# Optimization experiments

Measured on AMD Instinct MI355X. Metric: run time of the kernel, lower is better.

Reference implementation:

```python
import jax, jax.numpy as jnp
import numpy as np

N = 50000      # nodes
E = 400000     # edges
HID = 128      # hidden_size
L = 3          # num_att_layer
K = 9          # rbf_size
H = 4          # heads
C = HID // H   # out_channels per head (32)
G = 512        # graphs in batch
CUTOFF = 10.0


def _rbf(D):
    # ExponentialRBF: softplus(softplus_inverse(x)) == x, so centers/widths are the raw values
    centers = jnp.linspace(1.0, float(np.exp(-CUTOFF)), K)          # (K,)
    width = (0.5 / ((1.0 - np.exp(-CUTOFF)) / K)) ** 2              # scalar
    x = D / CUTOFF
    x3 = x ** 3
    x4 = x3 * x
    x5 = x4 * x
    cut = jnp.where(x < 1.0, 1.0 - 6.0 * x5 + 15.0 * x4 - 10.0 * x3, 0.0)
    return cut[:, None] * jnp.exp(-width * (jnp.exp(-D)[:, None] - centers) ** 2)  # (E,K)


def _ln(x, g, b):
    mu = jnp.mean(x, axis=-1, keepdims=True)
    var = jnp.var(x, axis=-1, keepdims=True)
    return (x - mu) / jnp.sqrt(var + 1e-5) * g + b


def _seg_softmax(logits, seg, n):
    # numerically stable softmax over edges grouped by target node
    m = jax.ops.segment_max(logits, seg, num_segments=n)
    e = jnp.exp(logits - m[seg])
    s = jax.ops.segment_sum(e, seg, num_segments=n)
    return e / s[seg]


def setup_inputs() -> dict:
    key = jax.random.key(0)
    ks = jax.random.split(key, 32)
    s = 1.0 / np.sqrt(HID)
    se = 1.0 / np.sqrt(K + 1)
    sb = 1.0 / np.sqrt(3 * HID)
    nrm = jax.random.normal
    inp = {
        "h": nrm(ks[0], (N, HID), jnp.float32),
        "pos": nrm(ks[1], (N, 3), jnp.float32) * 3.0,
        "edge_weight": jax.random.uniform(ks[2], (E,), jnp.float32),
        "Wq": nrm(ks[3], (L, HID, HID)) * s,   "bq": nrm(ks[4], (L, HID)) * 0.01,
        "Wk": nrm(ks[5], (L, HID, HID)) * s,   "bk": nrm(ks[6], (L, HID)) * 0.01,
        "Wv": nrm(ks[7], (L, HID, HID)) * s,   "bv": nrm(ks[8], (L, HID)) * 0.01,
        "We": nrm(ks[9], (L, K + 1, HID)) * se,
        "Wskip": nrm(ks[10], (L, HID, HID)) * s, "bskip": nrm(ks[11], (L, HID)) * 0.01,
        "Wbeta": nrm(ks[12], (L, 3 * HID, 1)) * sb,
        "Wffn1": nrm(ks[13], (L, HID, HID)) * s, "bffn1": nrm(ks[14], (L, HID)) * 0.01,
        "Wffn2": nrm(ks[15], (L, HID, HID)) * s, "bffn2": nrm(ks[16], (L, HID)) * 0.01,
        "Wffn3": nrm(ks[17], (L, HID, HID)) * s, "bffn3": nrm(ks[18], (L, HID)) * 0.01,
        "ln_g": jnp.ones((HID,), jnp.float32),
        "ln_b": jnp.zeros((HID,), jnp.float32),
        "Wo1": nrm(ks[19], (HID, HID)) * s, "bo1": nrm(ks[20], (HID,)) * 0.01,
        "Wo2": nrm(ks[21], (HID, 1)) * s,   "bo2": nrm(ks[22], (1,)) * 0.01,
        "edge_index": jax.random.randint(ks[23], (2, E), 0, N),
        "batch": jnp.sort(jax.random.randint(ks[24], (N,), 0, G)),
    }
    return inp


def reference(h, pos, edge_weight, Wq, bq, Wk, bk, Wv, bv, We, Wskip, bskip, Wbeta,
              Wffn1, bffn1, Wffn2, bffn2, Wffn3, bffn3, ln_g, ln_b, Wo1, bo1, Wo2, bo2,
              edge_index, batch):
    sp = jax.nn.softplus
    n = h.shape[0]
    src, dst = edge_index[0], edge_index[1]  # source j -> target i
    D = jnp.linalg.norm(pos[dst] - pos[src], axis=-1)              # (E,)
    efeat = jnp.concatenate([_rbf(D), edge_weight[:, None]], -1)   # (E, K+1)
    inv_sqrt_c = 1.0 / np.sqrt(C)

    for i in range(L):
        hn = _ln(h, ln_g, ln_b)
        q = (hn @ Wq[i] + bq[i]).reshape(n, H, C)
        k = (hn @ Wk[i] + bk[i]).reshape(n, H, C)
        v = (hn @ Wv[i] + bv[i]).reshape(n, H, C)
        ea = (efeat @ We[i]).reshape(-1, H, C)                     # (E,H,C)
        kj = k[src] + ea
        alpha = jnp.einsum('ehc,ehc->eh', q[dst], kj) * inv_sqrt_c  # (E,H)
        alpha = _seg_softmax(alpha, dst, n)
        # dropout p=0.5 is a no-op in eval mode
        msg = (v[src] + ea) * alpha[:, :, None]
        out = jax.ops.segment_sum(msg, dst, num_segments=n).reshape(n, H * C)
        x_r = hn @ Wskip[i] + bskip[i]
        beta = jax.nn.sigmoid(jnp.concatenate([out, x_r, out - x_r], -1) @ Wbeta[i])
        out = beta * x_r + (1.0 - beta) * out
        h = hn + sp(out)
        hn2 = _ln(h, ln_g, ln_b)
        f = sp(hn2 @ Wffn1[i] + bffn1[i])
        f = sp(f @ Wffn2[i] + bffn2[i])
        f = sp(f @ Wffn3[i] + bffn3[i])
        h = hn2 + f

    pooled = jax.ops.segment_sum(h, batch, num_segments=G)          # (G, HID)
    return sp(pooled @ Wo1 + bo1) @ Wo2 + bo2                       # (G, 1)
```

## Files before the change

kernel.cpp:

```cpp
#include <hip/hip_runtime.h>
#include <hip/hip_bf16.h>
#include <math.h>

#define HID 128
#define KRBF 9
#define NLAYER 3
#define IPAD 136

typedef __attribute__((ext_vector_type(8))) short bf16x8;
typedef __attribute__((ext_vector_type(4))) float f32x4;

__device__ __forceinline__ float sp_(float x){ return fmaxf(x,0.f) + log1pf(expf(-fabsf(x))); }
__device__ __forceinline__ float sigm_(float x){ return 1.f/(1.f+expf(-x)); }
__device__ __forceinline__ float b2f(short s){
  union{unsigned u; float f;} x; x.u = ((unsigned)(unsigned short)s)<<16; return x.f;
}
__device__ __forceinline__ short f2bs(float x){
  __hip_bfloat16 b = __float2bfloat16(x);
  return *reinterpret_cast<short*>(&b);
}
__device__ __forceinline__ float wsum64(float v){
  #pragma unroll
  for(int m=1;m<64;m<<=1) v += __shfl_xor(v,m,64);
  return v;
}
__device__ __forceinline__ float wsum16(float v){
  #pragma unroll
  for(int m=1;m<16;m<<=1) v += __shfl_xor(v,m,64);
  return v;
}
__device__ __forceinline__ int lb_(const int* __restrict__ a, int n, int key){
  int lo=0, hi=n;
  while(lo<hi){ int mid=(lo+hi)>>1; if(a[mid]<key) lo=mid+1; else hi=mid; }
  return lo;
}

__global__ void count_dst(const int* __restrict__ ei, int* __restrict__ counts, int E){
  int e = blockIdx.x*256+threadIdx.x;
  if(e<E) atomicAdd(&counts[ei[E+e]],1);
}
__global__ void scan1(const int* __restrict__ counts, int* __restrict__ tmp,
                      int* __restrict__ bsums, int N){
  __shared__ int lds[256];
  int t = threadIdx.x; int idx = blockIdx.x*256+t;
  int v = (idx<N)? counts[idx]:0;
  lds[t]=v; __syncthreads();
  for(int off=1;off<256;off<<=1){
    int x = (t>=off)? lds[t-off]:0;
    __syncthreads();
    lds[t]+=x; __syncthreads();
  }
  if(idx<N) tmp[idx]=lds[t];
  if(t==255) bsums[blockIdx.x]=lds[255];
}
__global__ void scan2(const int* __restrict__ bsums, int* __restrict__ boffs, int nb){
  __shared__ int lds[256];
  int t=threadIdx.x;
  int v = (t<nb)? bsums[t]:0;
  lds[t]=v; __syncthreads();
  for(int off=1;off<256;off<<=1){
    int x=(t>=off)?lds[t-off]:0;
    __syncthreads();
    lds[t]+=x; __syncthreads();
  }
  if(t<nb) boffs[t] = lds[t]-v;
}
__global__ void finalize_rs(const int* __restrict__ tmp, const int* __restrict__ boffs,
                            int* __restrict__ row_start, int N){
  int idx = blockIdx.x*256+threadIdx.x;
  if(idx<N) row_start[idx+1] = tmp[idx] + boffs[idx>>8];
  if(idx==0) row_start[0]=0;
}
__global__ void csr_scatter(const int* __restrict__ ei, const int* __restrict__ rowst,
                            int* __restrict__ counts2, int* __restrict__ csr, int E){
  int e = blockIdx.x*256+threadIdx.x;
  if(e>=E) return;
  int d = ei[E+e];
  int p = rowst[d] + atomicAdd(&counts2[d],1);
  csr[p] = e;
}
__global__ void sort_seg(const int* __restrict__ rowst, int* __restrict__ csr, int N){
  int n = blockIdx.x*256+threadIdx.x;
  if(n>=N) return;
  int lo=rowst[n], hi=rowst[n+1];
  for(int i=lo+1;i<hi;i++){
    int v=csr[i]; int j=i-1;
    while(j>=lo && csr[j]>v){ csr[j+1]=csr[j]; j--; }
    csr[j+1]=v;
  }
}
__global__ void edge_feat(const float* __restrict__ pos, const float* __restrict__ ew,
                          const int* __restrict__ ei, const int* __restrict__ csr,
                          float* __restrict__ efs, int* __restrict__ esrc, int E){
  int p = blockIdx.x*256 + threadIdx.x;
  if(p>=E) return;
  int e = csr[p];
  int s = ei[e], d = ei[E+e];
  float dx = pos[d*3+0]-pos[s*3+0];
  float dy = pos[d*3+1]-pos[s*3+1];
  float dz = pos[d*3+2]-pos[s*3+2];
  float D = sqrtf(dx*dx+dy*dy+dz*dz);
  float x = D*0.1f;
  float cut = 0.f;
  if(x < 1.f){ float x3=x*x*x, x4=x3*x, x5=x4*x; cut = 1.f - 6.f*x5 + 15.f*x4 - 10.f*x3; }
  float ed = expf(-D);
  const double e10 = 4.5399929762484854e-05;
  const float step  = (float)((e10 - 1.0)/8.0);
  const float width = (float)((4.5/(1.0-e10))*(4.5/(1.0-e10)));
  float r12[12];
  #pragma unroll
  for(int k=0;k<KRBF;k++){
    float c = 1.0f + k*step;
    float dd = ed - c;
    r12[k] = cut*expf(-width*dd*dd);
  }
  r12[9] = ew[e]; r12[10]=0.f; r12[11]=0.f;
  float* o = efs + (size_t)p*12;
  *(float4*)&o[0] = *(float4*)&r12[0];
  *(float4*)&o[4] = *(float4*)&r12[4];
  *(float4*)&o[8] = *(float4*)&r12[8];
  esrc[p] = s;
}

__global__ void pack_w(const float* __restrict__ Wq, const float* __restrict__ Wk,
                       const float* __restrict__ Wv, const float* __restrict__ Wsk,
                       const float* __restrict__ bq, const float* __restrict__ bk,
                       const float* __restrict__ bv, const float* __restrict__ bsk,
                       const float* __restrict__ We,
                       const float* __restrict__ W1, const float* __restrict__ W2,
                       const float* __restrict__ W3,
                       __hip_bfloat16* __restrict__ Wqkvs, float* __restrict__ bqkvs,
                       __hip_bfloat16* __restrict__ Wffn){
  int idx = blockIdx.x*256 + threadIdx.x;
  const int QT = NLAYER*5*16384;
  const int FT = NLAYER*3*16384;
  const int BT = NLAYER*640;
  if(idx < QT){
    int l = idx / (5*16384);
    int rem = idx - l*(5*16384);
    int cb = rem >> 14;
    int t = rem & 16383;
    int j = t&7; int lane = (t>>3)&63; int blk = t>>9;
    int kc = blk>>3, nj = blk&7, ql = lane>>4, il = lane&15;
    int k = kc*32 + ql*8 + j;
    int gcol = cb*128 + il*8 + nj;
    float v = 0.f;
    if(gcol < 512){
      const float* src = (gcol<128)?Wq:((gcol<256)?Wk:((gcol<384)?Wv:Wsk));
      v = src[(size_t)l*16384 + k*128 + (gcol&127)];
    } else if(gcol < 552){
      int jj = gcol-512; int h=jj/10; int r=jj-10*h;
      const float* wq = Wq + (size_t)l*16384 + k*128;
      const float* we = We + (size_t)l*1280 + r*128;
      float acc=0.f;
      #pragma unroll 8
      for(int c=32*h;c<32*h+32;c++) acc = fmaf(wq[c], we[c], acc);
      v = acc;
    }
    Wqkvs[idx] = __float2bfloat16(v);
  } else if(idx < QT+FT){
    int r0 = idx - QT;
    int l = r0 / (3*16384);
    int rem = r0 - l*(3*16384);
    int f = rem >> 14;
    int t = rem & 16383;
    int j = t&7; int lane = (t>>3)&63; int blk = t>>9;
    int kc = blk>>3, nj = blk&7, ql = lane>>4, il = lane&15;
    int k = kc*32 + ql*8 + j;
    int gcol = il*8 + nj;
    const float* src = (f==0)?W1:((f==1)?W2:W3);
    Wffn[r0] = __float2bfloat16(src[(size_t)l*16384 + k*128 + gcol]);
  } else if(idx < QT+FT+BT){
    int j = idx - QT - FT;
    int l = j/640; int col = j - l*640;
    float v = 0.f;
    if(col<512){
      const float* src = (col<128)?bq:((col<256)?bk:((col<384)?bv:bsk));
      v = src[l*128 + (col&127)];
    } else if(col<552){
      int jj=col-512; int h=jj/10; int r=jj-10*h;
      const float* bqp = bq + l*128;
      const float* we = We + (size_t)l*1280 + r*128;
      float acc=0.f;
      for(int c=32*h;c<32*h+32;c++) acc = fmaf(bqp[c], we[c], acc);
      v = acc;
    }
    bqkvs[j] = v;
  }
}

__global__ void ln_node(const float* __restrict__ h, const float* __restrict__ g,
                        const float* __restrict__ b, __hip_bfloat16* __restrict__ hn, int N){
  int n = blockIdx.x*4 + (threadIdx.x>>6);
  if(n>=N) return;
  int lane = threadIdx.x & 63;
  int c = 2*lane;
  float2 v = *(const float2*)&h[(size_t)n*HID + c];
  float s1 = wsum64(v.x+v.y);
  float s2 = wsum64(v.x*v.x+v.y*v.y);
  float mu = s1*(1.f/HID);
  float var = s2*(1.f/HID) - mu*mu;
  float rs = rsqrtf(var + 1e-5f);
  __hip_bfloat162 o;
  o.x = __float2bfloat16((v.x-mu)*rs*g[c]   + b[c]);
  o.y = __float2bfloat16((v.y-mu)*rs*g[c+1] + b[c+1]);
  *(__hip_bfloat162*)&hn[(size_t)n*HID + c] = o;
}

__global__ __launch_bounds__(256) void gemm_qkvs(
    const __hip_bfloat16* __restrict__ A, const __hip_bfloat16* __restrict__ Wt,
    const float* __restrict__ bias,
    __hip_bfloat16* __restrict__ qsO, __hip_bfloat16* __restrict__ kvO,
    float* __restrict__ qwO, int N){
  __shared__ __hip_bfloat16 WsF[16384];
  int row0 = blockIdx.y*128;
  int cb = blockIdx.x;
  int tid = threadIdx.x;
  {
    const __hip_bfloat16* Wp = Wt + (size_t)cb*16384;
    #pragma unroll
    for(int i=0;i<8;i++){
      int o = (tid + 256*i)*8;
      *(float4*)&WsF[o] = *(const float4*)&Wp[o];
    }
  }
  int lane = tid&63;
  int m0 = (tid>>6)*32;
  int ql = lane>>4, il = lane&15;
  bf16x8 af[2][4];
  #pragma unroll
  for(int mi=0;mi<2;mi++){
    int r = row0 + m0 + mi*16 + il;
    r = (r < N) ? r : (N-1);
    const __hip_bfloat16* ap = A + (size_t)r*128 + ql*8;
    #pragma unroll
    for(int kc=0;kc<4;kc++) af[mi][kc] = *(const bf16x8*)(ap + kc*32);
  }
  __syncthreads();
  f32x4 acc[2][8];
  #pragma unroll
  for(int mi=0;mi<2;mi++)
    #pragma unroll
    for(int nj=0;nj<8;nj++) acc[mi][nj] = (f32x4){0.f,0.f,0.f,0.f};
  #pragma unroll
  for(int kc=0;kc<4;kc++){
    #pragma unroll
    for(int nj=0;nj<8;nj++){
      bf16x8 bb = *(bf16x8*)&WsF[((kc*8+nj)*64 + lane)*8];
      #pragma unroll
      for(int mi=0;mi<2;mi++)
        acc[mi][nj] = __builtin_amdgcn_mfma_f32_16x16x32_bf16(af[mi][kc], bb, acc[mi][nj], 0,0,0);
    }
  }
  float bl8[8];
  {
    float4 b0 = *(const float4*)&bias[cb*128 + il*8];
    float4 b1 = *(const float4*)&bias[cb*128 + il*8 + 4];
    bl8[0]=b0.x; bl8[1]=b0.y; bl8[2]=b0.z; bl8[3]=b0.w;
    bl8[4]=b1.x; bl8[5]=b1.y; bl8[6]=b1.z; bl8[7]=b1.w;
  }
  #pragma unroll
  for(int mi=0;mi<2;mi++){
    #pragma unroll
    for(int r=0;r<4;r++){
      int rr = row0 + m0 + mi*16 + ql*4 + r;
      if(rr >= N) continue;
      if(cb < 4){
        bf16x8 o;
        #pragma unroll
        for(int nj=0;nj<8;nj++) o[nj] = f2bs(acc[mi][nj][r] + bl8[nj]);
        __hip_bfloat16* dst;
        if(cb==0)      dst = qsO + (size_t)rr*256 + il*8;
        else if(cb==1) dst = kvO + (size_t)rr*256 + il*8;
        else if(cb==2) dst = kvO + (size_t)rr*256 + 128 + il*8;
        else           dst = qsO + (size_t)rr*256 + 128 + il*8;
        *(bf16x8*)dst = o;
      } else if(il < 5){
        #pragma unroll
        for(int nj=0;nj<8;nj++){
          int g = il*8 + nj;
          int h = g/10, rb = g - 10*h;
          qwO[(size_t)rr*48 + h*12 + rb] = acc[mi][nj][r] + bl8[nj];
        }
      }
    }
  }
}

__global__ __launch_bounds__(256) void attn_fused4(
    const __hip_bfloat16* __restrict__ qs, const __hip_bfloat16* __restrict__ kvb,
    const float* __restrict__ qwb, const float* __restrict__ efs,
    const int* __restrict__ esrc, const float* __restrict__ WeL,
    const int* __restrict__ rowst, const __hip_bfloat16* __restrict__ hn,
    const float* __restrict__ Wb, const float* __restrict__ lng,
    const float* __restrict__ lnb, __hip_bfloat16* __restrict__ hn2, int N){
  int n = blockIdx.x*4 + (threadIdx.x>>6);
  if(n>=N) return;
  int lane = threadIdx.x & 63;
  int eg = lane>>4, sl = lane&15;
  int c8 = sl*8, hd = sl>>2;
  const __hip_bfloat16* rowq = qs + (size_t)n*256;
  float q8[8];
  {
    bf16x8 qv = *(const bf16x8*)&rowq[c8];
    #pragma unroll
    for(int j=0;j<8;j++) q8[j] = b2f(qv[j]);
  }
  const float* qwp = qwb + (size_t)n*48 + hd*12;
  float4 qa = *(const float4*)qwp;
  float4 qb = *(const float4*)(qwp+4);
  float2 qc = *(const float2*)(qwp+8);
  float QW[10] = {qa.x,qa.y,qa.z,qa.w,qb.x,qb.y,qb.z,qb.w,qc.x,qc.y};
  int lo = rowst[n], hi = rowst[n+1];
  float ssum = 0.f, a8[8], S[10];
  #pragma unroll
  for(int j=0;j<8;j++) a8[j]=0.f;
  #pragma unroll
  for(int r=0;r<10;r++) S[r]=0.f;
  int i = lo + eg;
  if(i < hi){
    int s = esrc[i];
    const __hip_bfloat16* kr = kvb + (size_t)s*256;
    bf16x8 kc = *(const bf16x8*)&kr[c8];
    bf16x8 vc = *(const bf16x8*)&kr[128 + c8];
    const float* ef = efs + (size_t)i*12;
    float4 e0 = *(const float4*)&ef[0];
    float4 e1 = *(const float4*)&ef[4];
    float2 e2 = *(const float2*)&ef[8];
    while(true){
      int inext = i + 4;
      bool more = inext < hi;
      bf16x8 kn = kc, vn = vc;
      float4 f0 = e0, f1 = e1; float2 f2 = e2;
      if(more){
        int s2 = esrc[inext];
        const __hip_bfloat16* kr2 = kvb + (size_t)s2*256;
        kn = *(const bf16x8*)&kr2[c8];
        vn = *(const bf16x8*)&kr2[128 + c8];
        const float* ef2 = efs + (size_t)inext*12;
        f0 = *(const float4*)&ef2[0];
        f1 = *(const float4*)&ef2[4];
        f2 = *(const float2*)&ef2[8];
      }
      float d = 0.f;
      #pragma unroll
      for(int j=0;j<8;j++) d = fmaf(q8[j], b2f(kc[j]), d);
      d += __shfl_xor(d,1,64); d += __shfl_xor(d,2,64);
      float lg = d;
      lg = fmaf(e0.x,QW[0],lg); lg = fmaf(e0.y,QW[1],lg);
      lg = fmaf(e0.z,QW[2],lg); lg = fmaf(e0.w,QW[3],lg);
      lg = fmaf(e1.x,QW[4],lg); lg = fmaf(e1.y,QW[5],lg);
      lg = fmaf(e1.z,QW[6],lg); lg = fmaf(e1.w,QW[7],lg);
      lg = fmaf(e2.x,QW[8],lg); lg = fmaf(e2.y,QW[9],lg);
      lg *= 0.17677669529663687f;
      lg = fminf(lg, 80.f);
      float w = __expf(lg);
      ssum += w;
      #pragma unroll
      for(int j=0;j<8;j++) a8[j] = fmaf(w, b2f(vc[j]), a8[j]);
      S[0]=fmaf(w,e0.x,S[0]); S[1]=fmaf(w,e0.y,S[1]); S[2]=fmaf(w,e0.z,S[2]);
      S[3]=fmaf(w,e0.w,S[3]); S[4]=fmaf(w,e1.x,S[4]); S[5]=fmaf(w,e1.y,S[5]);
      S[6]=fmaf(w,e1.z,S[6]); S[7]=fmaf(w,e1.w,S[7]); S[8]=fmaf(w,e2.x,S[8]);
      S[9]=fmaf(w,e2.y,S[9]);
      if(!more) break;
      kc = kn; vc = vn; e0 = f0; e1 = f1; e2 = f2;
      i = inext;
    }
  }
  float o8[8];
  #pragma unroll
  for(int j=0;j<8;j++) o8[j]=a8[j];
  #pragma unroll
  for(int r=0;r<10;r++){
    float s=S[r];
    float4 wa = *(const float4*)&WeL[r*128+c8];
    float4 wb = *(const float4*)&WeL[r*128+c8+4];
    o8[0]=fmaf(s,wa.x,o8[0]); o8[1]=fmaf(s,wa.y,o8[1]);
    o8[2]=fmaf(s,wa.z,o8[2]); o8[3]=fmaf(s,wa.w,o8[3]);
    o8[4]=fmaf(s,wb.x,o8[4]); o8[5]=fmaf(s,wb.y,o8[5]);
    o8[6]=fmaf(s,wb.z,o8[6]); o8[7]=fmaf(s,wb.w,o8[7]);
  }
  #pragma unroll
  for(int m=16;m<64;m<<=1){
    ssum += __shfl_xor(ssum,m,64);
    #pragma unroll
    for(int j=0;j<8;j++) o8[j] += __shfl_xor(o8[j],m,64);
  }
  float inv = (hi>lo)? 1.f/ssum : 0.f;
  #pragma unroll
  for(int j=0;j<8;j++) o8[j] *= inv;
  float xr8[8];
  {
    bf16x8 xv = *(const bf16x8*)&rowq[128 + c8];
    #pragma unroll
    for(int j=0;j<8;j++) xr8[j] = b2f(xv[j]);
  }
  float pb = 0.f;
  {
    float4 a0=*(const float4*)&Wb[c8],     a1=*(const float4*)&Wb[c8+4];
    float4 b0=*(const float4*)&Wb[128+c8], b1=*(const float4*)&Wb[128+c8+4];
    float4 c0=*(const float4*)&Wb[256+c8], c1=*(const float4*)&Wb[256+c8+4];
    float wb0[8]={a0.x,a0.y,a0.z,a0.w,a1.x,a1.y,a1.z,a1.w};
    float wb1[8]={b0.x,b0.y,b0.z,b0.w,b1.x,b1.y,b1.z,b1.w};
    float wb2[8]={c0.x,c0.y,c0.z,c0.w,c1.x,c1.y,c1.z,c1.w};
    #pragma unroll
    for(int j=0;j<8;j++)
      pb += o8[j]*wb0[j] + xr8[j]*wb1[j] + (o8[j]-xr8[j])*wb2[j];
  }
  pb = wsum16(pb);
  float beta = sigm_(pb);
  float h8[8], s1=0.f, s2=0.f;
  {
    bf16x8 hv = *(const bf16x8*)&hn[(size_t)n*128 + c8];
    #pragma unroll
    for(int j=0;j<8;j++){
      float u = beta*xr8[j] + (1.f-beta)*o8[j];
      float x = b2f(hv[j]) + sp_(u);
      h8[j]=x; s1+=x; s2+=x*x;
    }
  }
  s1 = wsum16(s1); s2 = wsum16(s2);
  float mu = s1*(1.f/128.f);
  float var = s2*(1.f/128.f) - mu*mu;
  float rsg = rsqrtf(var + 1e-5f);
  if(eg==0){
    float4 g0=*(const float4*)&lng[c8], g1=*(const float4*)&lng[c8+4];
    float4 bb0=*(const float4*)&lnb[c8], bb1=*(const float4*)&lnb[c8+4];
    float g8[8]={g0.x,g0.y,g0.z,g0.w,g1.x,g1.y,g1.z,g1.w};
    float lb8[8]={bb0.x,bb0.y,bb0.z,bb0.w,bb1.x,bb1.y,bb1.z,bb1.w};
    bf16x8 o;
    #pragma unroll
    for(int j=0;j<8;j++) o[j] = f2bs((h8[j]-mu)*rsg*g8[j] + lb8[j]);
    *(bf16x8*)&hn2[(size_t)n*128 + c8] = o;
  }
}

__global__ __launch_bounds__(256) void ffn_fused(
    const __hip_bfloat16* __restrict__ hn2, const __hip_bfloat16* __restrict__ Wf,
    const float* __restrict__ b1, const float* __restrict__ b2,
    const float* __restrict__ b3, const float* __restrict__ lng,
    const float* __restrict__ lnb, float* __restrict__ hout,
    __hip_bfloat16* __restrict__ hnout, int N){
  __shared__ __hip_bfloat16 WsF[16384];
  __shared__ __hip_bfloat16 inter[2][64][IPAD];
  int row0 = blockIdx.x*64;
  int tid = threadIdx.x, lane = tid&63, wv = tid>>6;
  int ql = lane>>4, il = lane&15;

  auto stage = [&](const __hip_bfloat16* Wp){
    #pragma unroll
    for(int i=0;i<8;i++){
      int o = (tid + 256*i)*8;
      *(float4*)&WsF[o] = *(const float4*)&Wp[o];
    }
  };
  auto loadbias = [&](const float* bp, float* bl8){
    float4 x0 = *(const float4*)&bp[il*8];
    float4 x1 = *(const float4*)&bp[il*8+4];
    bl8[0]=x0.x; bl8[1]=x0.y; bl8[2]=x0.z; bl8[3]=x0.w;
    bl8[4]=x1.x; bl8[5]=x1.y; bl8[6]=x1.z; bl8[7]=x1.w;
  };

  f32x4 acc[8];
  bf16x8 af[4];
  stage(Wf);
  {
    int r = row0 + wv*16 + il;
    r = (r<N)? r : (N-1);
    const __hip_bfloat16* ap = hn2 + (size_t)r*128 + ql*8;
    #pragma unroll
    for(int kc=0;kc<4;kc++) af[kc] = *(const bf16x8*)(ap + kc*32);
  }
  __syncthreads();
  #pragma unroll
  for(int nj=0;nj<8;nj++) acc[nj] = (f32x4){0.f,0.f,0.f,0.f};
  #pragma unroll
  for(int kc=0;kc<4;kc++)
    #pragma unroll
    for(int nj=0;nj<8;nj++){
      bf16x8 bb = *(bf16x8*)&WsF[((kc*8+nj)*64 + lane)*8];
      acc[nj] = __builtin_amdgcn_mfma_f32_16x16x32_bf16(af[kc], bb, acc[nj], 0,0,0);
    }
  {
    float bl8[8]; loadbias(b1, bl8);
    #pragma unroll
    for(int r=0;r<4;r++){
      int lr = wv*16 + ql*4 + r;
      bf16x8 o;
      #pragma unroll
      for(int nj=0;nj<8;nj++) o[nj] = f2bs(sp_(acc[nj][r] + bl8[nj]));
      *(bf16x8*)&inter[0][lr][il*8] = o;
    }
  }
  __syncthreads();
  stage(Wf + 16384);
  #pragma unroll
  for(int kc=0;kc<4;kc++) af[kc] = *(bf16x8*)&inter[0][wv*16+il][ql*8 + kc*32];
  __syncthreads();
  #pragma unroll
  for(int nj=0;nj<8;nj++) acc[nj] = (f32x4){0.f,0.f,0.f,0.f};
  #pragma unroll
  for(int kc=0;kc<4;kc++)
    #pragma unroll
    for(int nj=0;nj<8;nj++){
      bf16x8 bb = *(bf16x8*)&WsF[((kc*8+nj)*64 + lane)*8];
      acc[nj] = __builtin_amdgcn_mfma_f32_16x16x32_bf16(af[kc], bb, acc[nj], 0,0,0);
    }
  {
    float bl8[8]; loadbias(b2, bl8);
    #pragma unroll
    for(int r=0;r<4;r++){
      int lr = wv*16 + ql*4 + r;
      bf16x8 o;
      #pragma unroll
      for(int nj=0;nj<8;nj++) o[nj] = f2bs(sp_(acc[nj][r] + bl8[nj]));
      *(bf16x8*)&inter[1][lr][il*8] = o;
    }
  }
  __syncthreads();
  stage(Wf + 2*16384);
  #pragma unroll
  for(int kc=0;kc<4;kc++) af[kc] = *(bf16x8*)&inter[1][wv*16+il][ql*8 + kc*32];
  __syncthreads();
  #pragma unroll
  for(int nj=0;nj<8;nj++) acc[nj] = (f32x4){0.f,0.f,0.f,0.f};
  #pragma unroll
  for(int kc=0;kc<4;kc++)
    #pragma unroll
    for(int nj=0;nj<8;nj++){
      bf16x8 bb = *(bf16x8*)&WsF[((kc*8+nj)*64 + lane)*8];
      acc[nj] = __builtin_amdgcn_mfma_f32_16x16x32_bf16(af[kc], bb, acc[nj], 0,0,0);
    }
  {
    float bl8[8]; loadbias(b3, bl8);
    float lg8[8], lb8[8];
    loadbias(lng, lg8); loadbias(lnb, lb8);
    #pragma unroll
    for(int r=0;r<4;r++){
      int rr = row0 + wv*16 + ql*4 + r;
      if(rr >= N) continue;
      bf16x8 rv = *(const bf16x8*)&hn2[(size_t)rr*128 + il*8];
      float t8[8], s1=0.f, s2=0.f;
      #pragma unroll
      for(int nj=0;nj<8;nj++){
        float x = sp_(acc[nj][r] + bl8[nj]) + b2f(rv[nj]);
        t8[nj]=x; s1+=x; s2+=x*x;
      }
      s1 = wsum16(s1); s2 = wsum16(s2);
      float mu = s1*(1.f/128.f);
      float var = s2*(1.f/128.f) - mu*mu;
      float rsg = rsqrtf(var + 1e-5f);
      *(float4*)&hout[(size_t)rr*128 + il*8]     = make_float4(t8[0],t8[1],t8[2],t8[3]);
      *(float4*)&hout[(size_t)rr*128 + il*8 + 4] = make_float4(t8[4],t8[5],t8[6],t8[7]);
      bf16x8 o;
      #pragma unroll
      for(int nj=0;nj<8;nj++) o[nj] = f2bs((t8[nj]-mu)*rsg*lg8[nj] + lb8[nj]);
      *(bf16x8*)&hnout[(size_t)rr*128 + il*8] = o;
    }
  }
}

__global__ void pool_head(const float* __restrict__ h, const int* __restrict__ batch,
                          const float* __restrict__ Wo1, const float* __restrict__ bo1,
                          const float* __restrict__ Wo2, const float* __restrict__ bo2,
                          float* __restrict__ out, int N){
  int gid = blockIdx.x;
  int t = threadIdx.x;
  int lo = lb_(batch, N, gid), hi = lb_(batch, N, gid+1);
  __shared__ float pl[128];
  __shared__ float red[128];
  float s = 0.f;
  for(int i=lo;i<hi;i++) s += h[(size_t)i*HID + t];
  pl[t] = s;
  __syncthreads();
  float acc = bo1[t];
  for(int c=0;c<128;c++) acc = fmaf(pl[c], Wo1[c*HID+t], acc);
  red[t] = sp_(acc)*Wo2[t];
  __syncthreads();
  for(int off=64;off>0;off>>=1){
    if(t<off) red[t]+=red[t+off];
    __syncthreads();
  }
  if(t==0) out[gid] = red[0] + bo2[0];
}

extern "C" void kernel_launch(void* const* d_in, const int* in_sizes, int n_in,
                              void* d_out, int out_size, void* d_ws, size_t ws_size,
                              hipStream_t stream){
  const float* h_in = (const float*)d_in[0];
  const float* pos  = (const float*)d_in[1];
  const float* ew   = (const float*)d_in[2];
  const float* Wq = (const float*)d_in[3];  const float* bq = (const float*)d_in[4];
  const float* Wk = (const float*)d_in[5];  const float* bk = (const float*)d_in[6];
  const float* Wv = (const float*)d_in[7];  const float* bv = (const float*)d_in[8];
  const float* We = (const float*)d_in[9];
  const float* Wsk= (const float*)d_in[10]; const float* bsk=(const float*)d_in[11];
  const float* Wbeta=(const float*)d_in[12];
  const float* W1=(const float*)d_in[13]; const float* b1=(const float*)d_in[14];
  const float* W2=(const float*)d_in[15]; const float* b2=(const float*)d_in[16];
  const float* W3=(const float*)d_in[17]; const float* b3=(const float*)d_in[18];
  const float* lng=(const float*)d_in[19]; const float* lnb=(const float*)d_in[20];
  const float* Wo1=(const float*)d_in[21]; const float* bo1=(const float*)d_in[22];
  const float* Wo2=(const float*)d_in[23]; const float* bo2=(const float*)d_in[24];
  const int* ei    = (const int*)d_in[25];
  const int* batch = (const int*)d_in[26];
  int N = in_sizes[0]/HID;
  int E = in_sizes[2];
  int G = out_size;
  float* out = (float*)d_out;

  char* ws = (char*)d_ws;
  size_t off=0;
  auto alloc=[&](size_t bytes)->char*{
    char* p = ws + off;
    off = (off + bytes + 255) & ~(size_t)255;
    return p;
  };
  float* efs   =(float*)alloc((size_t)E*12*4);
  int* esrc    =(int*)  alloc((size_t)E*4);
  int* csr     =(int*)  alloc((size_t)E*4);
  int* counts  =(int*)  alloc((size_t)N*4);
  int* counts2 =(int*)  alloc((size_t)N*4);
  int* rowst   =(int*)  alloc((size_t)(N+1)*4);
  int* tmp     =(int*)  alloc((size_t)N*4);
  int* bsums   =(int*)  alloc(256*4);
  int* boffs   =(int*)  alloc(256*4);
  __hip_bfloat16* hn   =(__hip_bfloat16*)alloc((size_t)N*HID*2);
  __hip_bfloat16* hn2  =(__hip_bfloat16*)alloc((size_t)N*HID*2);
  __hip_bfloat16* qsb  =(__hip_bfloat16*)alloc((size_t)N*256*2);
  __hip_bfloat16* kvb  =(__hip_bfloat16*)alloc((size_t)N*256*2);
  float* qwb   =(float*)alloc((size_t)N*48*4);
  float* hcur  =(float*)alloc((size_t)N*HID*4);
  __hip_bfloat16* Wqkvs_t =(__hip_bfloat16*)alloc((size_t)NLAYER*5*16384*2);
  __hip_bfloat16* Wffn_t  =(__hip_bfloat16*)alloc((size_t)NLAYER*3*16384*2);
  float* bqkvs =(float*)alloc((size_t)NLAYER*640*4);

  int ebl = (E+255)/256;
  int nb  = (N+255)/256;
  int nwb = (N+3)/4;
  int nrb128 = (N+127)/128;
  int nrb64  = (N+63)/64;
  dim3 gqkvs(5, nrb128);

  hipMemsetAsync(counts, 0, (size_t)N*4, stream);
  hipMemsetAsync(counts2,0, (size_t)N*4, stream);
  count_dst<<<ebl,256,0,stream>>>(ei,counts,E);
  scan1<<<nb,256,0,stream>>>(counts,tmp,bsums,N);
  scan2<<<1,256,0,stream>>>(bsums,boffs,nb);
  finalize_rs<<<nb,256,0,stream>>>(tmp,boffs,rowst,N);
  csr_scatter<<<ebl,256,0,stream>>>(ei,rowst,counts2,csr,E);
  sort_seg<<<nb,256,0,stream>>>(rowst,csr,N);
  edge_feat<<<ebl,256,0,stream>>>(pos,ew,ei,csr,efs,esrc,E);
  {
    int tot = NLAYER*5*16384 + NLAYER*3*16384 + NLAYER*640;
    pack_w<<<(tot+255)/256,256,0,stream>>>(Wq,Wk,Wv,Wsk,bq,bk,bv,bsk,We,W1,W2,W3,
                                           Wqkvs_t,bqkvs,Wffn_t);
  }

  ln_node<<<nwb,256,0,stream>>>(h_in,lng,lnb,hn,N);
  for(int l=0;l<NLAYER;l++){
    const float* We_l = We + (size_t)l*(KRBF+1)*HID;
    const float* Wb_l = Wbeta + (size_t)l*3*HID;
    const float* b1_l = b1 + (size_t)l*HID;
    const float* b2_l = b2 + (size_t)l*HID;
    const float* b3_l = b3 + (size_t)l*HID;

    gemm_qkvs<<<gqkvs,256,0,stream>>>(hn, Wqkvs_t + (size_t)l*5*16384,
                                      bqkvs + l*640, qsb, kvb, qwb, N);
    attn_fused4<<<nwb,256,0,stream>>>(qsb,kvb,qwb,efs,esrc,We_l,rowst,hn,
                                      Wb_l,lng,lnb,hn2,N);
    ffn_fused<<<nrb64,256,0,stream>>>(hn2, Wffn_t + (size_t)l*3*16384,
                                      b1_l,b2_l,b3_l,lng,lnb,hcur,hn,N);
  }
  pool_head<<<G,128,0,stream>>>(hcur,batch,Wo1,bo1,Wo2,bo2,out,N);
}
```

Before: 926.7 us.

## Split attention epilogue into separate combine+LayerNorm kernel and drop software prefetch

The attention kernel now only aggregates messages and writes the normalized fp32 attention output. The beta gating, softplus residual and LayerNorm move into a new combine_ln kernel. The double-buffered prefetch loop is replaced by a simple strided loop, which is meant to lower register pressure and raise occupancy in the gather-heavy kernel. In exchange there is an extra fp32 N×128 round trip through memory and one more launch per layer, and the whole workspace is now memset instead of just the two count arrays.

```diff
diff --git a/kernel.cpp b/kernel.cpp
--- a/kernel.cpp
+++ b/kernel.cpp
@@ -28,6 +28,10 @@
   #pragma unroll
   for(int m=1;m<16;m<<=1) v += __shfl_xor(v,m,64);
   return v;
+}
+__device__ __forceinline__ float2 ldbf2(const __hip_bfloat16* p){
+  __hip_bfloat162 b = *(const __hip_bfloat162*)p;
+  return make_float2(__bfloat162float(b.x), __bfloat162float(b.y));
 }
 __device__ __forceinline__ int lb_(const int* __restrict__ a, int n, int key){
   int lo=0, hi=n;
@@ -287,13 +291,11 @@
   }
 }
 
-__global__ __launch_bounds__(256) void attn_fused4(
+__global__ __launch_bounds__(256) void attn_fused6(
     const __hip_bfloat16* __restrict__ qs, const __hip_bfloat16* __restrict__ kvb,
     const float* __restrict__ qwb, const float* __restrict__ efs,
     const int* __restrict__ esrc, const float* __restrict__ WeL,
-    const int* __restrict__ rowst, const __hip_bfloat16* __restrict__ hn,
-    const float* __restrict__ Wb, const float* __restrict__ lng,
-    const float* __restrict__ lnb, __hip_bfloat16* __restrict__ hn2, int N){
+    const int* __restrict__ rowst, float* __restrict__ att, int N){
   int n = blockIdx.x*4 + (threadIdx.x>>6);
   if(n>=N) return;
   int lane = threadIdx.x & 63;
@@ -317,8 +319,7 @@
   for(int j=0;j<8;j++) a8[j]=0.f;
   #pragma unroll
   for(int r=0;r<10;r++) S[r]=0.f;
-  int i = lo + eg;
-  if(i < hi){
+  for(int i=lo+eg; i<hi; i+=4){
     int s = esrc[i];
     const __hip_bfloat16* kr = kvb + (size_t)s*256;
     bf16x8 kc = *(const bf16x8*)&kr[c8];
@@ -327,45 +328,26 @@
     float4 e0 = *(const float4*)&ef[0];
     float4 e1 = *(const float4*)&ef[4];
     float2 e2 = *(const float2*)&ef[8];
-    while(true){
-      int inext = i + 4;
-      bool more = inext < hi;
-      bf16x8 kn = kc, vn = vc;
-      float4 f0 = e0, f1 = e1; float2 f2 = e2;
-      if(more){
-        int s2 = esrc[inext];
-        const __hip_bfloat16* kr2 = kvb + (size_t)s2*256;
-        kn = *(const bf16x8*)&kr2[c8];
-        vn = *(const bf16x8*)&kr2[128 + c8];
-        const float* ef2 = efs + (size_t)inext*12;
-        f0 = *(const float4*)&ef2[0];
-        f1 = *(const float4*)&ef2[4];
-        f2 = *(const float2*)&ef2[8];
-      }
-      float d = 0.f;
-      #pragma unroll
-      for(int j=0;j<8;j++) d = fmaf(q8[j], b2f(kc[j]), d);
-      d += __shfl_xor(d,1,64); d += __shfl_xor(d,2,64);
-      float lg = d;
-      lg = fmaf(e0.x,QW[0],lg); lg = fmaf(e0.y,QW[1],lg);
-      lg = fmaf(e0.z,QW[2],lg); lg = fmaf(e0.w,QW[3],lg);
-      lg = fmaf(e1.x,QW[4],lg); lg = fmaf(e1.y,QW[5],lg);
-      lg = fmaf(e1.z,QW[6],lg); lg = fmaf(e1.w,QW[7],lg);
-      lg = fmaf(e2.x,QW[8],lg); lg = fmaf(e2.y,QW[9],lg);
-      lg *= 0.17677669529663687f;
-      lg = fminf(lg, 80.f);
-      float w = __expf(lg);
-      ssum += w;
-      #pragma unroll
-      for(int j=0;j<8;j++) a8[j] = fmaf(w, b2f(vc[j]), a8[j]);
-      S[0]=fmaf(w,e0.x,S[0]); S[1]=fmaf(w,e0.y,S[1]); S[2]=fmaf(w,e0.z,S[2]);
-      S[3]=fmaf(w,e0.w,S[3]); S[4]=fmaf(w,e1.x,S[4]); S[5]=fmaf(w,e1.y,S[5]);
-      S[6]=fmaf(w,e1.z,S[6]); S[7]=fmaf(w,e1.w,S[7]); S[8]=fmaf(w,e2.x,S[8]);
-      S[9]=fmaf(w,e2.y,S[9]);
-      if(!more) break;
-      kc = kn; vc = vn; e0 = f0; e1 = f1; e2 = f2;
-      i = inext;
-    }
+    float d = 0.f;
+    #pragma unroll
+    for(int j=0;j<8;j++) d = fmaf(q8[j], b2f(kc[j]), d);
+    d += __shfl_xor(d,1,64); d += __shfl_xor(d,2,64);
+    float lg = d;
+    lg = fmaf(e0.x,QW[0],lg); lg = fmaf(e0.y,QW[1],lg);
+    lg = fmaf(e0.z,QW[2],lg); lg = fmaf(e0.w,QW[3],lg);
+    lg = fmaf(e1.x,QW[4],lg); lg = fmaf(e1.y,QW[5],lg);
+    lg = fmaf(e1.z,QW[6],lg); lg = fmaf(e1.w,QW[7],lg);
+    lg = fmaf(e2.x,QW[8],lg); lg = fmaf(e2.y,QW[9],lg);
+    lg *= 0.17677669529663687f;
+    lg = fminf(lg, 80.f);
+    float w = __expf(lg);
+    ssum += w;
+    #pragma unroll
+    for(int j=0;j<8;j++) a8[j] = fmaf(w, b2f(vc[j]), a8[j]);
+    S[0]=fmaf(w,e0.x,S[0]); S[1]=fmaf(w,e0.y,S[1]); S[2]=fmaf(w,e0.z,S[2]);
+    S[3]=fmaf(w,e0.w,S[3]); S[4]=fmaf(w,e1.x,S[4]); S[5]=fmaf(w,e1.y,S[5]);
+    S[6]=fmaf(w,e1.z,S[6]); S[7]=fmaf(w,e1.w,S[7]); S[8]=fmaf(w,e2.x,S[8]);
+    S[9]=fmaf(w,e2.y,S[9]);
   }
   float o8[8];
   #pragma unroll
@@ -386,53 +368,44 @@
     #pragma unroll
     for(int j=0;j<8;j++) o8[j] += __shfl_xor(o8[j],m,64);
   }
-  float inv = (hi>lo)? 1.f/ssum : 0.f;
-  #pragma unroll
-  for(int j=0;j<8;j++) o8[j] *= inv;
-  float xr8[8];
-  {
-    bf16x8 xv = *(const bf16x8*)&rowq[128 + c8];
-    #pragma unroll
-    for(int j=0;j<8;j++) xr8[j] = b2f(xv[j]);
-  }
-  float pb = 0.f;
-  {
-    float4 a0=*(const float4*)&Wb[c8],     a1=*(const float4*)&Wb[c8+4];
-    float4 b0=*(const float4*)&Wb[128+c8], b1=*(const float4*)&Wb[128+c8+4];
-    float4 c0=*(const float4*)&Wb[256+c8], c1=*(const float4*)&Wb[256+c8+4];
-    float wb0[8]={a0.x,a0.y,a0.z,a0.w,a1.x,a1.y,a1.z,a1.w};
-    float wb1[8]={b0.x,b0.y,b0.z,b0.w,b1.x,b1.y,b1.z,b1.w};
-    float wb2[8]={c0.x,c0.y,c0.z,c0.w,c1.x,c1.y,c1.z,c1.w};
-    #pragma unroll
-    for(int j=0;j<8;j++)
-      pb += o8[j]*wb0[j] + xr8[j]*wb1[j] + (o8[j]-xr8[j])*wb2[j];
-  }
-  pb = wsum16(pb);
-  float beta = sigm_(pb);
-  float h8[8], s1=0.f, s2=0.f;
-  {
-    bf16x8 hv = *(const bf16x8*)&hn[(size_t)n*128 + c8];
-    #pragma unroll
-    for(int j=0;j<8;j++){
-      float u = beta*xr8[j] + (1.f-beta)*o8[j];
-      float x = b2f(hv[j]) + sp_(u);
-      h8[j]=x; s1+=x; s2+=x*x;
-    }
-  }
-  s1 = wsum16(s1); s2 = wsum16(s2);
-  float mu = s1*(1.f/128.f);
-  float var = s2*(1.f/128.f) - mu*mu;
-  float rsg = rsqrtf(var + 1e-5f);
   if(eg==0){
-    float4 g0=*(const float4*)&lng[c8], g1=*(const float4*)&lng[c8+4];
-    float4 bb0=*(const float4*)&lnb[c8], bb1=*(const float4*)&lnb[c8+4];
-    float g8[8]={g0.x,g0.y,g0.z,g0.w,g1.x,g1.y,g1.z,g1.w};
-    float lb8[8]={bb0.x,bb0.y,bb0.z,bb0.w,bb1.x,bb1.y,bb1.z,bb1.w};
-    bf16x8 o;
-    #pragma unroll
-    for(int j=0;j<8;j++) o[j] = f2bs((h8[j]-mu)*rsg*g8[j] + lb8[j]);
-    *(bf16x8*)&hn2[(size_t)n*128 + c8] = o;
-  }
+    float inv = (hi>lo)? 1.f/ssum : 0.f;
+    float4 v0 = make_float4(o8[0]*inv, o8[1]*inv, o8[2]*inv, o8[3]*inv);
+    float4 v1 = make_float4(o8[4]*inv, o8[5]*inv, o8[6]*inv, o8[7]*inv);
+    *(float4*)&att[(size_t)n*128 + c8]     = v0;
+    *(float4*)&att[(size_t)n*128 + c8 + 4] = v1;
+  }
+}
+
+__global__ void combine_ln(const float* __restrict__ att, const __hip_bfloat16* __restrict__ qs,
+                           const __hip_bfloat16* __restrict__ hn, const float* __restrict__ Wb,
+                           const float* __restrict__ g, const float* __restrict__ b,
+                           __hip_bfloat16* __restrict__ hn2, int N){
+  int n = blockIdx.x*4 + (threadIdx.x>>6);
+  if(n>=N) return;
+  int lane = threadIdx.x&63;
+  int c = 2*lane;
+  float2 o  = *(const float2*)&att[(size_t)n*HID+c];
+  float2 xr = ldbf2(&qs[(size_t)n*256 + 128 + c]);
+  float bl = o.x*Wb[c] + o.y*Wb[c+1]
+           + xr.x*Wb[HID+c] + xr.y*Wb[HID+c+1]
+           + (o.x-xr.x)*Wb[2*HID+c] + (o.y-xr.y)*Wb[2*HID+c+1];
+  bl = wsum64(bl);
+  float beta = sigm_(bl);
+  float u0 = beta*xr.x + (1.f-beta)*o.x;
+  float u1 = beta*xr.y + (1.f-beta)*o.y;
+  float2 hnv = ldbf2(&hn[(size_t)n*HID+c]);
+  float h0 = hnv.x + sp_(u0);
+  float h1 = hnv.y + sp_(u1);
+  float s1 = wsum64(h0+h1);
+  float s2 = wsum64(h0*h0+h1*h1);
+  float mu = s1*(1.f/HID);
+  float var = s2*(1.f/HID)-mu*mu;
+  float rs = rsqrtf(var+1e-5f);
+  __hip_bfloat162 outv;
+  outv.x = __float2bfloat16((h0-mu)*rs*g[c]+b[c]);
+  outv.y = __float2bfloat16((h1-mu)*rs*g[c+1]+b[c+1]);
+  *(__hip_bfloat162*)&hn2[(size_t)n*HID+c] = outv;
 }
 
 __global__ __launch_bounds__(256) void ffn_fused(
@@ -630,10 +603,12 @@
   __hip_bfloat16* qsb  =(__hip_bfloat16*)alloc((size_t)N*256*2);
   __hip_bfloat16* kvb  =(__hip_bfloat16*)alloc((size_t)N*256*2);
   float* qwb   =(float*)alloc((size_t)N*48*4);
+  float* att   =(float*)alloc((size_t)N*HID*4);
   float* hcur  =(float*)alloc((size_t)N*HID*4);
   __hip_bfloat16* Wqkvs_t =(__hip_bfloat16*)alloc((size_t)NLAYER*5*16384*2);
   __hip_bfloat16* Wffn_t  =(__hip_bfloat16*)alloc((size_t)NLAYER*3*16384*2);
   float* bqkvs =(float*)alloc((size_t)NLAYER*640*4);
+  size_t ws_used = off;
 
   int ebl = (E+255)/256;
   int nb  = (N+255)/256;
@@ -642,8 +617,8 @@
   int nrb64  = (N+63)/64;
   dim3 gqkvs(5, nrb128);
 
-  hipMemsetAsync(counts, 0, (size_t)N*4, stream);
-  hipMemsetAsync(counts2,0, (size_t)N*4, stream);
+  hipMemsetAsync(ws, 0, (ws_used <= ws_size ? ws_used : ws_size), stream);
+
   count_dst<<<ebl,256,0,stream>>>(ei,counts,E);
   scan1<<<nb,256,0,stream>>>(counts,tmp,bsums,N);
   scan2<<<1,256,0,stream>>>(bsums,boffs,nb);
@@ -667,8 +642,8 @@
 
     gemm_qkvs<<<gqkvs,256,0,stream>>>(hn, Wqkvs_t + (size_t)l*5*16384,
                                       bqkvs + l*640, qsb, kvb, qwb, N);
-    attn_fused4<<<nwb,256,0,stream>>>(qsb,kvb,qwb,efs,esrc,We_l,rowst,hn,
-                                      Wb_l,lng,lnb,hn2,N);
+    attn_fused6<<<nwb,256,0,stream>>>(qsb,kvb,qwb,efs,esrc,We_l,rowst,att,N);
+    combine_ln<<<nwb,256,0,stream>>>(att,qsb,hn,Wb_l,lng,lnb,hn2,N);
     ffn_fused<<<nrb64,256,0,stream>>>(hn2, Wffn_t + (size_t)l*3*16384,
                                       b1_l,b2_l,b3_l,lng,lnb,hcur,hn,N);
   }
```

Result: faster. 883.1 us (-4.7%).
